# Kernel tuning notes

Measured on AMD Instinct MI355X. Metric: run time of the kernel, lower is better.

The kernel has to match this reference:

```python
import jax, jax.numpy as jnp
import numpy as np

B, H, S, D = 4, 16, 1024, 64
MAX_REL = 128
VOCAB = 2 * MAX_REL + 1  # relative-position vocabulary


def setup_inputs() -> dict:
    key = jax.random.key(0)
    k1, k2, k3, k4 = jax.random.split(key, 4)
    tensor = jax.random.normal(k1, (B, H, S, D), dtype=jnp.float32)
    rel_keys_emb = jax.random.normal(k2, (VOCAB, D), dtype=jnp.float32) * 0.02
    rel_values_emb = jax.random.normal(k3, (VOCAB, D), dtype=jnp.float32) * 0.02
    # nn.Parameter initialized xavier_uniform_ on shape (1, H, 1, 1)
    bias = jax.random.uniform(k4, (1, H, 1, 1), dtype=jnp.float32, minval=-1.0, maxval=1.0)
    return {
        "tensor": tensor,
        "rel_keys_emb": rel_keys_emb,
        "rel_values_emb": rel_values_emb,
        "bias": bias,
        "max_relative_position": MAX_REL,
    }


def reference(tensor, rel_keys_emb, rel_values_emb, bias, max_relative_position):
    # forward(tensor, is_key=True, transpose=False)
    seq_len = tensor.shape[2]
    r = jnp.arange(seq_len)
    dist = jnp.clip(r[None, :] - r[:, None], -max_relative_position, max_relative_position)
    idx = dist + max_relative_position          # [S, S] in [0, 2*max_rel]
    rel_emb = rel_keys_emb[idx]                 # [S, S, D] gathered table
    # original: [S, B*H, D] @ [S, D, S] -> [S, B*H, S] -> [B, H, S, S]
    scores = jnp.einsum('bhsd,std->bhst', tensor, rel_emb)
    return scores + bias
```

## Files before the change

### kernel.cpp

```cpp
#include <hip/hip_runtime.h>


constexpr int S_     = 1024;
constexpr int D_     = 64;
constexpr int BQ     = 64;
constexpr int CPITCH = 276;

typedef __attribute__((ext_vector_type(8))) short short8;
typedef __attribute__((ext_vector_type(4))) float f32x4;

__device__ __forceinline__ unsigned short f2bf(float x) {
  unsigned u = __float_as_uint(x);
  return (unsigned short)((u + 0x7fffu + ((u >> 16) & 1u)) >> 16);
}
__device__ __forceinline__ short8 pack8(float4 a, float4 b) {
  short8 r;
  r[0] = (short)f2bf(a.x); r[1] = (short)f2bf(a.y);
  r[2] = (short)f2bf(a.z); r[3] = (short)f2bf(a.w);
  r[4] = (short)f2bf(b.x); r[5] = (short)f2bf(b.y);
  r[6] = (short)f2bf(b.z); r[7] = (short)f2bf(b.w);
  return r;
}

__global__ __launch_bounds__(256, 4)
void relpos_v4(const float* __restrict__ tensor,
               const float* __restrict__ relk,
               const float* __restrict__ bias,
               float* __restrict__ out) {
  __shared__ __align__(16) unsigned short c_lds[BQ * CPITCH];

  const int tid  = threadIdx.x;
  const int lane = tid & 63;
  const int w    = tid >> 6;
  const int bh   = blockIdx.x >> 4;
  const int s0   = (blockIdx.x & 15) * BQ;
  const int h    = bh & 15;
  const int l15  = lane & 15;
  const int l4   = lane >> 4;
  const int r0   = 16 * w + l4 * 4;

  const float* xrow = tensor + ((size_t)(bh * S_ + s0 + 16 * w + l15)) * D_ + l4 * 8;
  short8 a0 = pack8(*reinterpret_cast<const float4*>(xrow),
                    *reinterpret_cast<const float4*>(xrow + 4));
  short8 a1 = pack8(*reinterpret_cast<const float4*>(xrow + 32),
                    *reinterpret_cast<const float4*>(xrow + 36));
  const float bv = bias[h];

#pragma unroll 2
  for (int nt = 0; nt < 17; ++nt) {
    const int vcol = 16 * nt + l15;
    const int erow = vcol > 256 ? 256 : vcol;
    const float* ep = relk + (size_t)erow * D_ + l4 * 8;
    short8 b0 = pack8(*reinterpret_cast<const float4*>(ep),
                      *reinterpret_cast<const float4*>(ep + 4));
    short8 b1 = pack8(*reinterpret_cast<const float4*>(ep + 32),
                      *reinterpret_cast<const float4*>(ep + 36));
    f32x4 acc = {0.f, 0.f, 0.f, 0.f};
    acc = __builtin_amdgcn_mfma_f32_16x16x32_bf16(a0, b0, acc, 0, 0, 0);
    acc = __builtin_amdgcn_mfma_f32_16x16x32_bf16(a1, b1, acc, 0, 0, 0);
    if (vcol <= 256) {
#pragma unroll
      for (int i = 0; i < 4; ++i) {
        c_lds[(r0 + i) * CPITCH + i + 4 + vcol] = f2bf(acc[i] + bv);
      }
    }
    if (l15 == 0 && nt == 0) {
#pragma unroll
      for (int i = 0; i < 4; ++i) {
        const unsigned short cv = f2bf(acc[i] + bv);
        for (int j = 0; j <= i + 3; ++j) c_lds[(r0 + i) * CPITCH + j] = cv;
      }
    }
    if (l15 == 0 && nt == 16) {
#pragma unroll
      for (int i = 0; i < 4; ++i) {
        const unsigned short cv = f2bf(acc[i] + bv);
        for (int j = i + 261; j < 268; ++j) c_lds[(r0 + i) * CPITCH + j] = cv;
      }
    }
  }
  __syncthreads();

  float* obase = out + ((size_t)bh * S_ + s0) * (size_t)S_;
  const int mc = 132 - s0;
#pragma unroll 4
  for (int it = 0; it < 64; ++it) {
    const int idx = it * 256 + tid;
    const int rl  = idx >> 8;
    const int t0  = (idx & 255) << 2;
    int m0 = t0 + (rl & 3) + mc - rl;
    m0 = m0 < 0 ? 0 : (m0 > 264 ? 264 : m0);
    const uint2 q = *reinterpret_cast<const uint2*>(&c_lds[rl * CPITCH + m0]);
    float4 o;
    o.x = __uint_as_float(q.x << 16);
    o.y = __uint_as_float(q.x & 0xffff0000u);
    o.z = __uint_as_float(q.y << 16);
    o.w = __uint_as_float(q.y & 0xffff0000u);
    *reinterpret_cast<float4*>(&obase[(size_t)idx * 4]) = o;
  }
}

extern "C" void kernel_launch(void* const* d_in, const int* in_sizes, int n_in,
                              void* d_out, int out_size, void* d_ws, size_t ws_size,
                              hipStream_t stream) {
  const float* tensor = (const float*)d_in[0];
  const float* relk   = (const float*)d_in[1];
  const float* bias   = (const float*)d_in[3];
  float* out          = (float*)d_out;

  const int B = 4, H = 16;
  dim3 grid(B * H * (S_ / BQ));
  dim3 block(256);
  relpos_v4<<<grid, block, 0, stream>>>(tensor, relk, bias, out);
}
```

Measured before the change: 73.66 us.

## Split compute and output expansion into two kernels via workspace

Splits the fused kernel in two. The first kernel computes the compact banded bf16 score table per block and writes it from LDS to a global workspace. A second, high-occupancy kernel then reads that table back and expands it into the full fp32 output with a different row-to-block mapping. The goal is to separate the MFMA/LDS phase from the bandwidth-bound store phase so stores are spread across more concurrent blocks, at the cost of an extra launch and an extra global round trip for the workspace.

```diff
diff --git a/kernel.cpp b/kernel.cpp
--- a/kernel.cpp
+++ b/kernel.cpp
@@ -23,10 +23,10 @@
 }
 
 __global__ __launch_bounds__(256, 4)
-void relpos_v4(const float* __restrict__ tensor,
-               const float* __restrict__ relk,
-               const float* __restrict__ bias,
-               float* __restrict__ out) {
+void relpos_c(const float* __restrict__ tensor,
+              const float* __restrict__ relk,
+              const float* __restrict__ bias,
+              unsigned short* __restrict__ c_ws) {
   __shared__ __align__(16) unsigned short c_lds[BQ * CPITCH];
 
   const int tid  = threadIdx.x;
@@ -60,9 +60,8 @@
     acc = __builtin_amdgcn_mfma_f32_16x16x32_bf16(a1, b1, acc, 0, 0, 0);
     if (vcol <= 256) {
 #pragma unroll
-      for (int i = 0; i < 4; ++i) {
+      for (int i = 0; i < 4; ++i)
         c_lds[(r0 + i) * CPITCH + i + 4 + vcol] = f2bf(acc[i] + bv);
-      }
     }
     if (l15 == 0 && nt == 0) {
 #pragma unroll
@@ -81,22 +80,35 @@
   }
   __syncthreads();
 
-  float* obase = out + ((size_t)bh * S_ + s0) * (size_t)S_;
-  const int mc = 132 - s0;
+  const uint4* src = reinterpret_cast<const uint4*>(c_lds);
+  uint4* dst = reinterpret_cast<uint4*>(c_ws + (size_t)blockIdx.x * (BQ * CPITCH));
+  constexpr int NV4 = BQ * CPITCH / 8;
+#pragma unroll
+  for (int i = 0; i < 9; ++i) {
+    int idx = tid + 256 * i;
+    if (idx < NV4) dst[idx] = src[idx];
+  }
+}
+
+__global__ __launch_bounds__(256, 8)
+void relpos_expand(const unsigned short* __restrict__ c_ws,
+                   float* __restrict__ out) {
+  const int tid = threadIdx.x;
+  const int bid = blockIdx.x;
+  const int t0  = tid << 2;
 #pragma unroll 4
-  for (int it = 0; it < 64; ++it) {
-    const int idx = it * 256 + tid;
-    const int rl  = idx >> 8;
-    const int t0  = (idx & 255) << 2;
-    int m0 = t0 + (rl & 3) + mc - rl;
+  for (int it = 0; it < 32; ++it) {
+    const int g = (it << 11) + bid;
+    const int s = g & (S_ - 1);
+    int m0 = t0 + (s & 3) + 132 - s;
     m0 = m0 < 0 ? 0 : (m0 > 264 ? 264 : m0);
-    const uint2 q = *reinterpret_cast<const uint2*>(&c_lds[rl * CPITCH + m0]);
+    const uint2 q = *reinterpret_cast<const uint2*>(&c_ws[(size_t)g * CPITCH + m0]);
     float4 o;
     o.x = __uint_as_float(q.x << 16);
     o.y = __uint_as_float(q.x & 0xffff0000u);
     o.z = __uint_as_float(q.y << 16);
     o.w = __uint_as_float(q.y & 0xffff0000u);
-    *reinterpret_cast<float4*>(&obase[(size_t)idx * 4]) = o;
+    *reinterpret_cast<float4*>(&out[((size_t)g << 10) + t0]) = o;
   }
 }
 
@@ -107,9 +119,8 @@
   const float* relk   = (const float*)d_in[1];
   const float* bias   = (const float*)d_in[3];
   float* out          = (float*)d_out;
+  unsigned short* c_ws = (unsigned short*)d_ws;
 
-  const int B = 4, H = 16;
-  dim3 grid(B * H * (S_ / BQ));
-  dim3 block(256);
-  relpos_v4<<<grid, block, 0, stream>>>(tensor, relk, bias, out);
+  relpos_c<<<dim3(1024), dim3(256), 0, stream>>>(tensor, relk, bias, c_ws);
+  relpos_expand<<<dim3(2048), dim3(256), 0, stream>>>(c_ws, out);
 }
```

Measured after the change: 130.3 us. 76.9% more time.
